# Kernel tuning notes

Hardware: AMD Instinct MI355X
Metric: run time of the kernel (lower is better)

Reference implementation:

```python
import jax, jax.numpy as jnp
import numpy as np

BETA = 0.25  # commitment_cost


def setup_inputs() -> dict:
    key = jax.random.key(0)
    k1, k2 = jax.random.split(key)
    B, T, K, D = 4096, 64, 512, 64
    z_e = jax.random.normal(k1, (B, T, D), dtype=jnp.float32)
    # torch init: uniform_(-1/K, 1/K) per slot codebook, stacked -> (T, K, D)
    codebooks = jax.random.uniform(k2, (T, K, D), dtype=jnp.float32,
                                   minval=-1.0 / K, maxval=1.0 / K)
    return {"z_e": z_e, "codebooks": codebooks}


def reference(z_e, codebooks):
    """ProductQuantizer.forward (use_ema=True, eval), vectorized over slots.

    z_e:       (B, T, D)
    codebooks: (T, K, D)
    Returns (z_q_st, tokens, vq_loss, utilization).
    """
    B, T, D = z_e.shape
    K = codebooks.shape[1]
    # squared-L2 distances per slot: (B, T, K)
    distances = (
        jnp.sum(z_e * z_e, axis=-1, keepdims=True)          # (B, T, 1)
        - 2.0 * jnp.einsum("btd,tkd->btk", z_e, codebooks)  # (B, T, K)
        + jnp.sum(codebooks * codebooks, axis=-1)[None]      # (1, T, K)
    )
    tokens = jnp.argmin(distances, axis=-1)                  # (B, T) int
    # gather nearest code per (batch, slot)
    z_q = codebooks[jnp.arange(T)[None, :], tokens]          # (B, T, D)
    # straight-through estimator
    z_q_st = z_e + jax.lax.stop_gradient(z_q - z_e)
    # use_ema=True branch: loss = mean_t( beta * mse(z_e_t, sg(z_q_t)) )
    # all slots have equal size, so this equals beta * global mean sq err
    vq_loss = BETA * jnp.mean(jnp.square(z_e - jax.lax.stop_gradient(z_q)))
    # utilization: fraction of (slot, code) pairs used at least once
    flat_idx = (jnp.arange(T)[None, :] * K + tokens).ravel()
    used = jnp.zeros((T * K,), dtype=z_e.dtype).at[flat_idx].set(1.0)
    utilization = jnp.sum(used) / (T * K)
    return z_q_st, tokens, vq_loss, utilization
```

## Files before the change

### kernel.cpp

```cpp
#include <hip/hip_runtime.h>

#define B_N 4096
#define T_N 64
#define K_N 512
#define D_N 64


__global__ __launch_bounds__(256) void zero_ws_kernel(unsigned* __restrict__ used,
                                                      double* __restrict__ loss) {
    int i = blockIdx.x * 256 + threadIdx.x;
    if (i < T_N * K_N) used[i] = 0u;
    if (i == 0) *loss = 0.0;
}

__global__ __launch_bounds__(256) void c2_kernel(const float* __restrict__ cb,
                                                 float* __restrict__ c2) {
    int i = blockIdx.x * 256 + threadIdx.x;
    if (i >= T_N * K_N) return;
    const float* c = cb + (size_t)i * D_N;
    float s = 0.0f;
#pragma unroll
    for (int d = 0; d < D_N; ++d) s = __fadd_rn(s, __fmul_rn(c[d], c[d]));
    c2[i] = s;
}

__global__ __launch_bounds__(256) void vq_main(const float* __restrict__ z_e,
                                               const float* __restrict__ cb,
                                               const float* __restrict__ c2,
                                               float* __restrict__ zq_out,
                                               float* __restrict__ tok_out,
                                               unsigned* __restrict__ used,
                                               double* __restrict__ loss_sum) {
    const int t = blockIdx.y;
    const int b = blockIdx.x * 256 + threadIdx.x;

    const float* zrow = z_e + ((size_t)b * T_N + t) * D_N;
    float z[D_N];
#pragma unroll
    for (int d4 = 0; d4 < D_N / 4; ++d4) {
        float4 v = reinterpret_cast<const float4*>(zrow)[d4];
        z[4 * d4 + 0] = v.x; z[4 * d4 + 1] = v.y;
        z[4 * d4 + 2] = v.z; z[4 * d4 + 3] = v.w;
    }

    float A = 0.0f;
#pragma unroll
    for (int d = 0; d < D_N; ++d) A = __fadd_rn(A, __fmul_rn(z[d], z[d]));

    const float* cbt = cb + (size_t)t * K_N * D_N;
    const float* c2t = c2 + t * K_N;

    float best = __builtin_inff();
    int tok = 0;
    for (int k = 0; k < K_N; ++k) {
        const float* ck = cbt + (size_t)k * D_N;
        float acc = 0.0f;
#pragma unroll
        for (int d = 0; d < D_N; ++d) acc = __builtin_fmaf(z[d], ck[d], acc);
        float dist = __fadd_rn(__fsub_rn(A, __fmul_rn(2.0f, acc)), c2t[k]);
        if (dist < best) { best = dist; tok = k; }
    }

    const float* q = cbt + (size_t)tok * D_N;
    float* zq = zq_out + ((size_t)b * T_N + t) * D_N;
    double ld = 0.0;
#pragma unroll
    for (int d4 = 0; d4 < D_N / 4; ++d4) {
        float4 qv = reinterpret_cast<const float4*>(q)[d4];
        reinterpret_cast<float4*>(zq)[d4] = qv;
        float d0 = z[4 * d4 + 0] - qv.x;
        float d1 = z[4 * d4 + 1] - qv.y;
        float d2 = z[4 * d4 + 2] - qv.z;
        float d3 = z[4 * d4 + 3] - qv.w;
        ld += (double)d0 * d0 + (double)d1 * d1 + (double)d2 * d2 + (double)d3 * d3;
    }
    tok_out[(size_t)b * T_N + t] = (float)tok;
    used[t * K_N + tok] = 1u;

    __shared__ double sred[256];
    sred[threadIdx.x] = ld;
    __syncthreads();
    for (int s = 128; s > 0; s >>= 1) {
        if (threadIdx.x < s) sred[threadIdx.x] += sred[threadIdx.x + s];
        __syncthreads();
    }
    if (threadIdx.x == 0) atomicAdd(loss_sum, sred[0]);
}

__global__ __launch_bounds__(512) void finalize_kernel(const unsigned* __restrict__ used,
                                                       const double* __restrict__ loss_sum,
                                                       float* __restrict__ out) {
    __shared__ unsigned s[512];
    unsigned c = 0;
    for (int i = threadIdx.x; i < T_N * K_N; i += 512) c += used[i];
    s[threadIdx.x] = c;
    __syncthreads();
    for (int st = 256; st > 0; st >>= 1) {
        if (threadIdx.x < st) s[threadIdx.x] += s[threadIdx.x + st];
        __syncthreads();
    }
    if (threadIdx.x == 0) {
        const size_t base = (size_t)B_N * T_N * D_N + (size_t)B_N * T_N;
        out[base]     = (float)(0.25 * (*loss_sum) / (double)((size_t)B_N * T_N * D_N));
        out[base + 1] = (float)s[0] / (float)(T_N * K_N);
    }
}

extern "C" void kernel_launch(void* const* d_in, const int* in_sizes, int n_in,
                              void* d_out, int out_size, void* d_ws, size_t ws_size,
                              hipStream_t stream) {
    const float* z_e = (const float*)d_in[0];
    const float* cb  = (const float*)d_in[1];
    float* out = (float*)d_out;

    float*    c2   = (float*)d_ws;
    unsigned* used = (unsigned*)((char*)d_ws + 131072);
    double*   loss = (double*)((char*)d_ws + 262144);

    zero_ws_kernel<<<128, 256, 0, stream>>>(used, loss);
    c2_kernel<<<128, 256, 0, stream>>>(cb, c2);

    float* tok_out = out + (size_t)B_N * T_N * D_N;
    vq_main<<<dim3(B_N / 256, T_N), 256, 0, stream>>>(z_e, cb, c2, out, tok_out, used, loss);

    finalize_kernel<<<1, 512, 0, stream>>>(used, loss, out);
}
```

Baseline: 455.9 us.

## Stage codebook chunks in double-buffered LDS and compute two rows per thread

```diff
diff --git a/kernel.cpp b/kernel.cpp
--- a/kernel.cpp
+++ b/kernel.cpp
@@ -4,98 +4,165 @@
 #define T_N 64
 #define K_N 512
 #define D_N 64
+#define KC 64
+#define NCHUNK (K_N / KC)
 
 
-__global__ __launch_bounds__(256) void zero_ws_kernel(unsigned* __restrict__ used,
-                                                      double* __restrict__ loss) {
+__global__ __launch_bounds__(256) void prep_kernel(const float* __restrict__ cb,
+                                                   float* __restrict__ c2,
+                                                   unsigned* __restrict__ used,
+                                                   double* __restrict__ loss) {
     int i = blockIdx.x * 256 + threadIdx.x;
-    if (i < T_N * K_N) used[i] = 0u;
+    used[i] = 0u;
     if (i == 0) *loss = 0.0;
-}
-
-__global__ __launch_bounds__(256) void c2_kernel(const float* __restrict__ cb,
-                                                 float* __restrict__ c2) {
-    int i = blockIdx.x * 256 + threadIdx.x;
-    if (i >= T_N * K_N) return;
-    const float* c = cb + (size_t)i * D_N;
+    const float4* c = reinterpret_cast<const float4*>(cb + (size_t)i * D_N);
     float s = 0.0f;
 #pragma unroll
-    for (int d = 0; d < D_N; ++d) s = __fadd_rn(s, __fmul_rn(c[d], c[d]));
+    for (int j = 0; j < 16; ++j) {
+        float4 v = c[j];
+        s = __fadd_rn(s, __fmul_rn(v.x, v.x));
+        s = __fadd_rn(s, __fmul_rn(v.y, v.y));
+        s = __fadd_rn(s, __fmul_rn(v.z, v.z));
+        s = __fadd_rn(s, __fmul_rn(v.w, v.w));
+    }
     c2[i] = s;
 }
 
-__global__ __launch_bounds__(256) void vq_main(const float* __restrict__ z_e,
-                                               const float* __restrict__ cb,
-                                               const float* __restrict__ c2,
-                                               float* __restrict__ zq_out,
-                                               float* __restrict__ tok_out,
-                                               unsigned* __restrict__ used,
-                                               double* __restrict__ loss_sum) {
-    const int t = blockIdx.y;
-    const int b = blockIdx.x * 256 + threadIdx.x;
+__global__ __launch_bounds__(256, 2) void vq_main(const float* __restrict__ z_e,
+                                                  const float* __restrict__ cb,
+                                                  const float* __restrict__ c2,
+                                                  float* __restrict__ zq_out,
+                                                  float* __restrict__ tok_out,
+                                                  unsigned* __restrict__ used,
+                                                  double* __restrict__ loss_sum) {
+    const int t   = blockIdx.y;
+    const int tid = threadIdx.x;
+    const int b0  = blockIdx.x * 512 + 2 * tid;
+    const int b1  = b0 + 1;
 
-    const float* zrow = z_e + ((size_t)b * T_N + t) * D_N;
-    float z[D_N];
+    __shared__ __align__(16) float cbuf[2][KC * D_N];
+    __shared__ __align__(16) float c2buf[2][KC];
+
+    float z0[D_N], z1[D_N];
+    const float* zr0 = z_e + ((size_t)b0 * T_N + t) * D_N;
+    const float* zr1 = z_e + ((size_t)b1 * T_N + t) * D_N;
 #pragma unroll
-    for (int d4 = 0; d4 < D_N / 4; ++d4) {
-        float4 v = reinterpret_cast<const float4*>(zrow)[d4];
-        z[4 * d4 + 0] = v.x; z[4 * d4 + 1] = v.y;
-        z[4 * d4 + 2] = v.z; z[4 * d4 + 3] = v.w;
+    for (int j = 0; j < 16; ++j) {
+        float4 v0 = reinterpret_cast<const float4*>(zr0)[j];
+        float4 v1 = reinterpret_cast<const float4*>(zr1)[j];
+        z0[4*j+0] = v0.x; z0[4*j+1] = v0.y; z0[4*j+2] = v0.z; z0[4*j+3] = v0.w;
+        z1[4*j+0] = v1.x; z1[4*j+1] = v1.y; z1[4*j+2] = v1.z; z1[4*j+3] = v1.w;
     }
 
-    float A = 0.0f;
+    float A0 = 0.0f, A1 = 0.0f;
 #pragma unroll
-    for (int d = 0; d < D_N; ++d) A = __fadd_rn(A, __fmul_rn(z[d], z[d]));
+    for (int d = 0; d < D_N; ++d) A0 = __fadd_rn(A0, __fmul_rn(z0[d], z0[d]));
+#pragma unroll
+    for (int d = 0; d < D_N; ++d) A1 = __fadd_rn(A1, __fmul_rn(z1[d], z1[d]));
 
     const float* cbt = cb + (size_t)t * K_N * D_N;
     const float* c2t = c2 + t * K_N;
 
-    float best = __builtin_inff();
-    int tok = 0;
-    for (int k = 0; k < K_N; ++k) {
-        const float* ck = cbt + (size_t)k * D_N;
-        float acc = 0.0f;
+    float4 pf[4];
+    float4 c2pf;
+
+    auto issue = [&](int c) {
+        const float4* src = reinterpret_cast<const float4*>(cbt + (size_t)c * KC * D_N);
 #pragma unroll
-        for (int d = 0; d < D_N; ++d) acc = __builtin_fmaf(z[d], ck[d], acc);
-        float dist = __fadd_rn(__fsub_rn(A, __fmul_rn(2.0f, acc)), c2t[k]);
-        if (dist < best) { best = dist; tok = k; }
+        for (int j = 0; j < 4; ++j) pf[j] = src[j * 256 + tid];
+        if (tid < 16) c2pf = reinterpret_cast<const float4*>(c2t + c * KC)[tid];
+    };
+    auto writebuf = [&](int buf) {
+#pragma unroll
+        for (int j = 0; j < 4; ++j) reinterpret_cast<float4*>(cbuf[buf])[j * 256 + tid] = pf[j];
+        if (tid < 16) reinterpret_cast<float4*>(c2buf[buf])[tid] = c2pf;
+    };
+
+    issue(0);
+    writebuf(0);
+    __syncthreads();
+
+    float best0 = __builtin_inff(), best1 = __builtin_inff();
+    int tok0 = 0, tok1 = 0;
+
+    for (int c = 0; c < NCHUNK; ++c) {
+        if (c < NCHUNK - 1) issue(c + 1);
+        const float* cc  = cbuf[c & 1];
+        const float* c2c = c2buf[c & 1];
+        for (int kk = 0; kk < KC; ++kk) {
+            const float* crow = cc + kk * D_N;
+            float a0 = 0.0f, a1 = 0.0f;
+#pragma unroll
+            for (int d = 0; d < D_N; ++d) {
+                float cd = crow[d];
+                a0 = __builtin_fmaf(z0[d], cd, a0);
+                a1 = __builtin_fmaf(z1[d], cd, a1);
+            }
+            float c2k = c2c[kk];
+            float dist0 = __fadd_rn(__fsub_rn(A0, __fmul_rn(2.0f, a0)), c2k);
+            float dist1 = __fadd_rn(__fsub_rn(A1, __fmul_rn(2.0f, a1)), c2k);
+            int k = c * KC + kk;
+            if (dist0 < best0) { best0 = dist0; tok0 = k; }
+            if (dist1 < best1) { best1 = dist1; tok1 = k; }
+        }
+        if (c < NCHUNK - 1) {
+            __syncthreads();
+            writebuf((c + 1) & 1);
+            __syncthreads();
+        }
     }
 
-    const float* q = cbt + (size_t)tok * D_N;
-    float* zq = zq_out + ((size_t)b * T_N + t) * D_N;
+    const float* q0 = cbt + (size_t)tok0 * D_N;
+    const float* q1 = cbt + (size_t)tok1 * D_N;
+    float* zq0 = zq_out + ((size_t)b0 * T_N + t) * D_N;
+    float* zq1 = zq_out + ((size_t)b1 * T_N + t) * D_N;
     double ld = 0.0;
 #pragma unroll
-    for (int d4 = 0; d4 < D_N / 4; ++d4) {
-        float4 qv = reinterpret_cast<const float4*>(q)[d4];
-        reinterpret_cast<float4*>(zq)[d4] = qv;
-        float d0 = z[4 * d4 + 0] - qv.x;
-        float d1 = z[4 * d4 + 1] - qv.y;
-        float d2 = z[4 * d4 + 2] - qv.z;
-        float d3 = z[4 * d4 + 3] - qv.w;
-        ld += (double)d0 * d0 + (double)d1 * d1 + (double)d2 * d2 + (double)d3 * d3;
+    for (int j = 0; j < 16; ++j) {
+        float4 qv = reinterpret_cast<const float4*>(q0)[j];
+        reinterpret_cast<float4*>(zq0)[j] = qv;
+        float d0 = z0[4*j+0] - qv.x, d1 = z0[4*j+1] - qv.y;
+        float d2 = z0[4*j+2] - qv.z, d3 = z0[4*j+3] - qv.w;
+        ld += (double)d0*d0 + (double)d1*d1 + (double)d2*d2 + (double)d3*d3;
     }
-    tok_out[(size_t)b * T_N + t] = (float)tok;
-    used[t * K_N + tok] = 1u;
+#pragma unroll
+    for (int j = 0; j < 16; ++j) {
+        float4 qv = reinterpret_cast<const float4*>(q1)[j];
+        reinterpret_cast<float4*>(zq1)[j] = qv;
+        float d0 = z1[4*j+0] - qv.x, d1 = z1[4*j+1] - qv.y;
+        float d2 = z1[4*j+2] - qv.z, d3 = z1[4*j+3] - qv.w;
+        ld += (double)d0*d0 + (double)d1*d1 + (double)d2*d2 + (double)d3*d3;
+    }
+    tok_out[(size_t)b0 * T_N + t] = (float)tok0;
+    tok_out[(size_t)b1 * T_N + t] = (float)tok1;
+    used[t * K_N + tok0] = 1u;
+    used[t * K_N + tok1] = 1u;
 
-    __shared__ double sred[256];
-    sred[threadIdx.x] = ld;
+    __syncthreads();
+    double* red = reinterpret_cast<double*>(cbuf[0]);
+    red[tid] = ld;
     __syncthreads();
     for (int s = 128; s > 0; s >>= 1) {
-        if (threadIdx.x < s) sred[threadIdx.x] += sred[threadIdx.x + s];
+        if (tid < s) red[tid] += red[tid + s];
         __syncthreads();
     }
-    if (threadIdx.x == 0) atomicAdd(loss_sum, sred[0]);
+    if (tid == 0) atomicAdd(loss_sum, red[0]);
 }
 
-__global__ __launch_bounds__(512) void finalize_kernel(const unsigned* __restrict__ used,
-                                                       const double* __restrict__ loss_sum,
-                                                       float* __restrict__ out) {
-    __shared__ unsigned s[512];
+__global__ __launch_bounds__(1024) void finalize_kernel(const unsigned* __restrict__ used,
+                                                        const double* __restrict__ loss_sum,
+                                                        float* __restrict__ out) {
+    __shared__ unsigned s[1024];
+    const uint4* u4 = reinterpret_cast<const uint4*>(used);
     unsigned c = 0;
-    for (int i = threadIdx.x; i < T_N * K_N; i += 512) c += used[i];
+#pragma unroll
+    for (int i = 0; i < 8; ++i) {
+        uint4 v = u4[threadIdx.x + i * 1024];
+        c += v.x + v.y + v.z + v.w;
+    }
     s[threadIdx.x] = c;
     __syncthreads();
-    for (int st = 256; st > 0; st >>= 1) {
+    for (int st = 512; st > 0; st >>= 1) {
         if (threadIdx.x < st) s[threadIdx.x] += s[threadIdx.x + st];
         __syncthreads();
     }
@@ -117,11 +184,10 @@
     unsigned* used = (unsigned*)((char*)d_ws + 131072);
     double*   loss = (double*)((char*)d_ws + 262144);
 
-    zero_ws_kernel<<<128, 256, 0, stream>>>(used, loss);
-    c2_kernel<<<128, 256, 0, stream>>>(cb, c2);
+    prep_kernel<<<128, 256, 0, stream>>>(cb, c2, used, loss);
 
     float* tok_out = out + (size_t)B_N * T_N * D_N;
-    vq_main<<<dim3(B_N / 256, T_N), 256, 0, stream>>>(z_e, cb, c2, out, tok_out, used, loss);
+    vq_main<<<dim3(B_N / 512, T_N), 256, 0, stream>>>(z_e, cb, c2, out, tok_out, used, loss);
 
-    finalize_kernel<<<1, 512, 0, stream>>>(used, loss, out);
+    finalize_kernel<<<1, 1024, 0, stream>>>(used, loss, out);
 }
```

New measurement: 399.6 us. -12.3%, faster.
